# Optimization experiments

Measured on AMD Instinct MI355X. Metric: run time of the kernel, lower is better.

The kernel has to match this reference:

```python
import jax, jax.numpy as jnp
import numpy as np

B, S, IK, IV = 16, 2048, 3, 1
D = IK + IV          # input_size = 4
H = 256              # hidden_size
F = 512              # dim_feedforward
L = 2                # num_layers
EPS = 1e-5


def setup_inputs() -> dict:
    key = jax.random.key(0)
    ks = jax.random.split(key, 16)
    n = jax.random.normal
    inp = {
        'KEY': n(ks[0], (B, S, IK), jnp.float32),
        'VALUE': n(ks[1], (B, S, IV), jnp.float32),
        # per-layer kernel-attention projections (stacked on layer axis)
        'Wq': n(ks[2], (L, D, H), jnp.float32) * 0.1,
        'bq': jnp.zeros((L, H), jnp.float32),
        'Wk': n(ks[3], (L, D, H), jnp.float32) * 0.1,
        'bk': jnp.zeros((L, H), jnp.float32),
        'Wv': n(ks[4], (L, D, H), jnp.float32) * 0.1,
        'bv': jnp.zeros((L, H), jnp.float32),
        'Wo': n(ks[5], (L, H, D), jnp.float32) * 0.1,
        'bo': jnp.zeros((L, D), jnp.float32),
        'bw': jnp.ones((L,), jnp.float32),          # Gaussian kernel bandwidth
        # LayerNorm 1
        'g1': jnp.ones((L, D), jnp.float32),
        'be1': jnp.zeros((L, D), jnp.float32),
        # FFN
        'W1': n(ks[6], (L, D, F), jnp.float32) * 0.1,
        'b1': jnp.zeros((L, F), jnp.float32),
        'W2': n(ks[7], (L, F, D), jnp.float32) * 0.1,
        'b2': jnp.zeros((L, D), jnp.float32),
        # LayerNorm 2
        'g2': jnp.ones((L, D), jnp.float32),
        'be2': jnp.zeros((L, D), jnp.float32),
        # final fc: input_size -> input_v
        'Wfc': n(ks[8], (D, IV), jnp.float32) * 0.1,
        'bfc': jnp.zeros((IV,), jnp.float32),
    }
    return inp


def _layernorm(x, g, b):
    m = x.mean(-1, keepdims=True)
    v = ((x - m) ** 2).mean(-1, keepdims=True)
    return (x - m) * jax.lax.rsqrt(v + EPS) * g + b


def reference(KEY, VALUE, Wq, bq, Wk, bk, Wv, bv, Wo, bo, bw,
              g1, be1, W1, b1, W2, b2, g2, be2, Wfc, bfc):
    # positioning: concat coords and values -> [B, S, D]
    X = jnp.concatenate([KEY, VALUE], axis=-1)
    n_layers = Wq.shape[0]
    for i in range(n_layers):
        # Nadaraya-Watson Gaussian kernel attention (madsnn, type='nwd', kernel='gauss')
        Q = X @ Wq[i] + bq[i]                      # [B,S,H]
        K = X @ Wk[i] + bk[i]                      # [B,S,H]
        V = X @ Wv[i] + bv[i]                      # [B,S,H]
        # pairwise squared distances ||q-k||^2, [B,S,S]
        d2 = ((Q * Q).sum(-1)[:, :, None]
              + (K * K).sum(-1)[:, None, :]
              - 2.0 * jnp.einsum('bqh,bkh->bqk', Q, K))
        attn = jax.nn.softmax(-0.5 * d2 * (bw[i] ** 2), axis=-1)
        attn_out = jnp.einsum('bqk,bkh->bqh', attn, V) @ Wo[i] + bo[i]  # [B,S,D]
        # residual + LayerNorm + FFN + residual + LayerNorm (dropout = identity in eval)
        res = _layernorm(X + attn_out, g1[i], be1[i])
        ff = jax.nn.relu(res @ W1[i] + b1[i]) @ W2[i] + b2[i]
        X = _layernorm(res + ff, g2[i], be2[i])
    return X @ Wfc + bfc                            # [B,S,IV]
```

## Files before the change

kernel.cpp:

```cpp
#include <hip/hip_runtime.h>

#define BB 16
#define SS 2048
#define NTOK (BB*SS)
#define FF 512
#define EPSF 1e-5f

#if __has_builtin(__builtin_amdgcn_exp2f)
#define EXP2F(x) __builtin_amdgcn_exp2f(x)
#else
#define EXP2F(x) exp2f(x)
#endif


__device__ __forceinline__ float wred64(float v) {
#pragma unroll
  for (int m = 32; m > 0; m >>= 1) v += __shfl_xor(v, m, 64);
  return v;
}


__global__ __launch_bounds__(64) void prep_kernel(
    const float* __restrict__ Wq, const float* __restrict__ bq,
    const float* __restrict__ Wk, const float* __restrict__ bk,
    const float* __restrict__ Wv, const float* __restrict__ bv,
    const float* __restrict__ Wo, const float* __restrict__ bw,
    const float* __restrict__ W1, const float* __restrict__ b1,
    const float* __restrict__ W2,
    float* __restrict__ sm, float* __restrict__ w1t)
{
  const int i = blockIdx.x;
  const int lane = threadIdx.x;
  float m4[4][4] = {{0}}, gkk[4][4] = {{0}}, wvo[4][4] = {{0}};
  float akk[4] = {0}, bvo[4] = {0};
  float ck1 = 0.f, ck2 = 0.f;

  for (int h = lane; h < 256; h += 64) {
    float vq[4], vk[4], vv[4], wo4[4];
#pragma unroll
    for (int a = 0; a < 4; ++a) {
      vq[a]  = Wq[(i*4 + a)*256 + h];
      vk[a]  = Wk[(i*4 + a)*256 + h];
      vv[a]  = Wv[(i*4 + a)*256 + h];
      wo4[a] = Wo[(i*256 + h)*4 + a];
    }
    const float bqh = bq[i*256 + h], bkh = bk[i*256 + h], bvh = bv[i*256 + h];
#pragma unroll
    for (int a = 0; a < 4; ++a) {
#pragma unroll
      for (int c = 0; c < 4; ++c) {
        m4[a][c]  = fmaf(vq[a], vk[c], m4[a][c]);
        gkk[a][c] = fmaf(vk[a], vk[c], gkk[a][c]);
        wvo[a][c] = fmaf(vv[a], wo4[c], wvo[a][c]);
      }
      akk[a] = fmaf(vk[a], bqh - bkh, akk[a]);
      bvo[a] = fmaf(bvh, wo4[a], bvo[a]);
    }
    ck1 = fmaf(bqh, bkh, ck1);
    ck2 = fmaf(bkh, bkh, ck2);
  }
#pragma unroll
  for (int a = 0; a < 4; ++a) {
#pragma unroll
    for (int c = 0; c < 4; ++c) {
      m4[a][c]  = wred64(m4[a][c]);
      gkk[a][c] = wred64(gkk[a][c]);
      wvo[a][c] = wred64(wvo[a][c]);
    }
    akk[a] = wred64(akk[a]);
    bvo[a] = wred64(bvo[a]);
  }
  ck1 = wred64(ck1); ck2 = wred64(ck2);

  if (lane == 0) {
    const float bwv = bw[i];
    const float bw2 = bwv * bwv * 1.44269504088896f;
    float* s = sm + i*64;
#pragma unroll
    for (int a = 0; a < 4; ++a) {
#pragma unroll
      for (int c = 0; c < 4; ++c) {
        s[a*4+c]      = bw2 * m4[a][c];
        s[16 + a*4+c] = -0.5f * bw2 * gkk[a][c];
        s[32 + a*4+c] = wvo[a][c];
      }
      s[48+a] = bw2 * akk[a];
      s[52+a] = bvo[a];
    }
    s[56] = bw2 * (ck1 - 0.5f * ck2);
  }
  for (int f = lane; f < FF; f += 64) {
    float* rec = w1t + (i*FF + f)*12;
#pragma unroll
    for (int c = 0; c < 4; ++c) rec[c]   = W1[(i*4 + c)*FF + f];
#pragma unroll
    for (int c = 0; c < 4; ++c) rec[4+c] = W2[(i*FF + f)*4 + c];
    rec[8] = b1[i*FF + f];
    rec[9] = 0.f; rec[10] = 0.f; rec[11] = 0.f;
  }
}

__device__ __forceinline__ void compute_feat(const float x[4], const float* __restrict__ s,
                                             float* __restrict__ featrec)
{
  float P[4], VT[4], tk[4];
#pragma unroll
  for (int a = 0; a < 4; ++a) {
    P[a]  = fmaf(s[a*4+3], x[3], fmaf(s[a*4+2], x[2], fmaf(s[a*4+1], x[1], s[a*4+0]*x[0])));
    tk[a] = fmaf(s[16+a*4+3], x[3], fmaf(s[16+a*4+2], x[2], fmaf(s[16+a*4+1], x[1], s[16+a*4+0]*x[0])));
    VT[a] = s[52+a] + fmaf(s[32+3*4+a], x[3], fmaf(s[32+2*4+a], x[2], fmaf(s[32+1*4+a], x[1], s[32+0*4+a]*x[0])));
  }
  float R = s[56];
#pragma unroll
  for (int a = 0; a < 4; ++a) R = fmaf(tk[a] + s[48+a], x[a], R);
  float4* fp = (float4*)featrec;
  fp[0] = make_float4(P[0], P[1], P[2], P[3]);
  fp[1] = make_float4(VT[0], VT[1], VT[2], VT[3]);
  fp[2] = make_float4(R, 0.f, 0.f, 0.f);
}

__global__ __launch_bounds__(256) void f0_kernel(
    const float* __restrict__ KEY, const float* __restrict__ VALUE,
    const float* __restrict__ sm, float* __restrict__ X0, float* __restrict__ feat)
{
  const int gq = blockIdx.x*256 + threadIdx.x;
  float x[4];
  x[0] = KEY[gq*3 + 0];
  x[1] = KEY[gq*3 + 1];
  x[2] = KEY[gq*3 + 2];
  x[3] = VALUE[gq];
  *(float4*)(X0 + (size_t)gq*4) = make_float4(x[0], x[1], x[2], x[3]);
  float fr[12];
  compute_feat(x, sm, fr);
  float4* fp = (float4*)(feat + (size_t)gq*12);
  fp[0] = ((float4*)fr)[0]; fp[1] = ((float4*)fr)[1]; fp[2] = ((float4*)fr)[2];
}

__global__ __launch_bounds__(256) void attn_kernel(
    const float* __restrict__ feat, const float* __restrict__ X,
    float* __restrict__ part)
{
  __shared__ float smem[512*21];
  const int bid = blockIdx.x;
  const int b = bid >> 5;
  const int r = bid & 31;
  const int qg = r >> 3, kb = r & 7;
  const int qbase = (b << 11) + (qg << 9);
  const int kbase = (b << 11) + (kb << 8);
  const int tid = threadIdx.x;
  const int lane = tid & 63, wave = tid >> 6;

  {
    const float4* src = (const float4*)(feat + (size_t)kbase*12);
    float4* dst = (float4*)smem;
    dst[tid] = src[tid];
    dst[tid + 256] = src[tid + 256];
    dst[tid + 512] = src[tid + 512];
  }

  float xq[8][4], acc[8][5];
#pragma unroll
  for (int j = 0; j < 8; ++j) {
    const float4 xv = *(const float4*)(X + (size_t)(qbase + j*64 + lane)*4);
    xq[j][0] = xv.x; xq[j][1] = xv.y; xq[j][2] = xv.z; xq[j][3] = xv.w;
#pragma unroll
    for (int c = 0; c < 5; ++c) acc[j][c] = 0.f;
  }
  __syncthreads();

  const float* kf = smem + wave*64*12;
#pragma unroll 2
  for (int k = 0; k < 64; ++k) {
    const float* kp = kf + k*12;
    const float4 P  = *(const float4*)kp;
    const float4 VT = *(const float4*)(kp + 4);
    const float R = kp[8];
#pragma unroll
    for (int j = 0; j < 8; ++j) {
      float l = fmaf(xq[j][3], P.w, fmaf(xq[j][2], P.z,
                fmaf(xq[j][1], P.y, fmaf(xq[j][0], P.x, R))));
      const float e = EXP2F(l);
      acc[j][0] = fmaf(e, VT.x, acc[j][0]);
      acc[j][1] = fmaf(e, VT.y, acc[j][1]);
      acc[j][2] = fmaf(e, VT.z, acc[j][2]);
      acc[j][3] = fmaf(e, VT.w, acc[j][3]);
      acc[j][4] += e;
    }
  }
  __syncthreads();
#pragma unroll
  for (int j = 0; j < 8; ++j) {
    float* rr = smem + (j*64 + lane)*21 + wave*5;
    rr[0] = acc[j][0]; rr[1] = acc[j][1]; rr[2] = acc[j][2];
    rr[3] = acc[j][3]; rr[4] = acc[j][4];
  }
  __syncthreads();
  float* pb = part + (size_t)kb * NTOK * 8;
#pragma unroll
  for (int t = 0; t < 2; ++t) {
    const int q = t*256 + tid;
    const float* rr = smem + q*21;
    float s0 = 0.f, s1 = 0.f, s2 = 0.f, s3 = 0.f, s4 = 0.f;
#pragma unroll
    for (int w = 0; w < 4; ++w) {
      s0 += rr[w*5+0]; s1 += rr[w*5+1]; s2 += rr[w*5+2];
      s3 += rr[w*5+3]; s4 += rr[w*5+4];
    }
    float* pp = pb + (size_t)(qbase + q)*8;
    *(float4*)pp = make_float4(s0, s1, s2, s3);
    pp[4] = s4;
  }
}

__device__ __forceinline__ void ln4(const float t[4], const float* __restrict__ g,
                                    const float* __restrict__ b, float r[4])
{
  const float m = 0.25f*(t[0]+t[1]+t[2]+t[3]);
  const float d0 = t[0]-m, d1 = t[1]-m, d2 = t[2]-m, d3 = t[3]-m;
  const float v = 0.25f*(d0*d0 + d1*d1 + d2*d2 + d3*d3);
  const float sc = rsqrtf(v + EPSF);
  r[0] = fmaf(d0*sc, g[0], b[0]);
  r[1] = fmaf(d1*sc, g[1], b[1]);
  r[2] = fmaf(d2*sc, g[2], b[2]);
  r[3] = fmaf(d3*sc, g[3], b[3]);
}

__global__ __launch_bounds__(512) void combine_kernel(
    const float* __restrict__ part, const float* __restrict__ Xin,
    const float* __restrict__ w1t,
    const float* __restrict__ bo, const float* __restrict__ g1, const float* __restrict__ be1,
    const float* __restrict__ b2v, const float* __restrict__ g2, const float* __restrict__ be2,
    const float* __restrict__ smn,
    float* __restrict__ Xout, float* __restrict__ feat,
    const float* __restrict__ Wfc, const float* __restrict__ bfc,
    float* __restrict__ outp, int last)
{
  const int tok = threadIdx.x & 63, fc = threadIdx.x >> 6;
  const int gq = blockIdx.x*64 + tok;
  __shared__ float redp[8][64][5];
  __shared__ float ress[64][4];
  __shared__ float redf[8][64][4];

  {
    const float* pp = part + ((size_t)fc*NTOK + gq)*8;
    const float4 v = *(const float4*)pp;
    redp[fc][tok][0] = v.x; redp[fc][tok][1] = v.y;
    redp[fc][tok][2] = v.z; redp[fc][tok][3] = v.w;
    redp[fc][tok][4] = pp[4];
  }
  __syncthreads();

  if (fc == 0) {
    float acc[5] = {0,0,0,0,0};
#pragma unroll
    for (int k = 0; k < 8; ++k)
#pragma unroll
      for (int c = 0; c < 5; ++c) acc[c] += redp[k][tok][c];
    const float inv = 1.0f / acc[4];
    const float4 xv = *(const float4*)(Xin + (size_t)gq*4);
    float t[4];
    t[0] = xv.x + fmaf(acc[0], inv, bo[0]);
    t[1] = xv.y + fmaf(acc[1], inv, bo[1]);
    t[2] = xv.z + fmaf(acc[2], inv, bo[2]);
    t[3] = xv.w + fmaf(acc[3], inv, bo[3]);
    float r[4];
    ln4(t, g1, be1, r);
    ress[tok][0] = r[0]; ress[tok][1] = r[1]; ress[tok][2] = r[2]; ress[tok][3] = r[3];
  }
  __syncthreads();

  const float r0 = ress[tok][0], r1 = ress[tok][1], r2 = ress[tok][2], r3 = ress[tok][3];
  float fa[4] = {0,0,0,0};
  const float* wt = w1t + (size_t)fc*64*12;
#pragma unroll 4
  for (int f = 0; f < 64; ++f) {
    const float* rec = wt + f*12;
    const float4 w1r = *(const float4*)rec;
    const float4 w2r = *(const float4*)(rec + 4);
    const float b1f = rec[8];
    float h = fmaf(r3, w1r.w, fmaf(r2, w1r.z, fmaf(r1, w1r.y, fmaf(r0, w1r.x, b1f))));
    h = fmaxf(h, 0.f);
    fa[0] = fmaf(h, w2r.x, fa[0]);
    fa[1] = fmaf(h, w2r.y, fa[1]);
    fa[2] = fmaf(h, w2r.z, fa[2]);
    fa[3] = fmaf(h, w2r.w, fa[3]);
  }
  redf[fc][tok][0] = fa[0]; redf[fc][tok][1] = fa[1];
  redf[fc][tok][2] = fa[2]; redf[fc][tok][3] = fa[3];
  __syncthreads();

  if (fc == 0) {
    float t2[4];
#pragma unroll
    for (int c = 0; c < 4; ++c) {
      float s = b2v[c];
#pragma unroll
      for (int k = 0; k < 8; ++k) s += redf[k][tok][c];
      t2[c] = ress[tok][c] + s;
    }
    float y[4];
    ln4(t2, g2, be2, y);
    if (last) {
      outp[gq] = fmaf(y[3], Wfc[3], fmaf(y[2], Wfc[2], fmaf(y[1], Wfc[1], fmaf(y[0], Wfc[0], bfc[0]))));
    } else {
      *(float4*)(Xout + (size_t)gq*4) = make_float4(y[0], y[1], y[2], y[3]);
      float fr[12];
      compute_feat(y, smn, fr);
      float4* fp = (float4*)(feat + (size_t)gq*12);
      fp[0] = ((float4*)fr)[0]; fp[1] = ((float4*)fr)[1]; fp[2] = ((float4*)fr)[2];
    }
  }
}

extern "C" void kernel_launch(void* const* d_in, const int* in_sizes, int n_in,
                              void* d_out, int out_size, void* d_ws, size_t ws_size,
                              hipStream_t stream)
{
  const float* KEY   = (const float*)d_in[0];
  const float* VALUE = (const float*)d_in[1];
  const float* Wq  = (const float*)d_in[2];
  const float* bq  = (const float*)d_in[3];
  const float* Wk  = (const float*)d_in[4];
  const float* bk  = (const float*)d_in[5];
  const float* Wv  = (const float*)d_in[6];
  const float* bv  = (const float*)d_in[7];
  const float* Wo  = (const float*)d_in[8];
  const float* bo  = (const float*)d_in[9];
  const float* bw  = (const float*)d_in[10];
  const float* g1  = (const float*)d_in[11];
  const float* be1 = (const float*)d_in[12];
  const float* W1  = (const float*)d_in[13];
  const float* b1  = (const float*)d_in[14];
  const float* W2  = (const float*)d_in[15];
  const float* b2  = (const float*)d_in[16];
  const float* g2  = (const float*)d_in[17];
  const float* be2 = (const float*)d_in[18];
  const float* Wfc = (const float*)d_in[19];
  const float* bfc = (const float*)d_in[20];
  float* out = (float*)d_out;

  float* w    = (float*)d_ws;
  float* sm   = w;
  float* w1t  = w + 128;
  float* feat = w + 12416;
  float* X0   = w + 405632;
  float* X1   = w + 536704;
  float* part = w + 667776;

  prep_kernel<<<2, 64, 0, stream>>>(Wq, bq, Wk, bk, Wv, bv, Wo, bw, W1, b1, W2, sm, w1t);
  f0_kernel<<<128, 256, 0, stream>>>(KEY, VALUE, sm, X0, feat);

  attn_kernel<<<512, 256, 0, stream>>>(feat, X0, part);
  combine_kernel<<<512, 512, 0, stream>>>(part, X0, w1t,
      bo, g1, be1, b2, g2, be2,
      sm + 64, X1, feat, Wfc, bfc, out, 0);

  attn_kernel<<<512, 256, 0, stream>>>(feat, X1, part);
  combine_kernel<<<512, 512, 0, stream>>>(part, X1, w1t + FF*12,
      bo + 4, g1 + 4, be1 + 4, b2 + 4, g2 + 4, be2 + 4,
      sm, X0, feat, Wfc, bfc, out, 1);
}
```

Before: 191.8 us.

## Compute key features on the fly in attention kernel, merge f0 into prep

Drops the precomputed per-token feature buffer. Each attention block now recomputes its 256 key features from X into shared memory, and the combine kernel no longer writes features. The f0 kernel is folded into prep_kernel, which also packs KEY/VALUE into X0, removing one launch. This trades a small amount of redundant per-block compute for less global memory traffic and one fewer kernel launch.

```diff
diff --git a/kernel.cpp b/kernel.cpp
--- a/kernel.cpp
+++ b/kernel.cpp
@@ -20,16 +20,25 @@
 }
 
 
-__global__ __launch_bounds__(64) void prep_kernel(
+__global__ __launch_bounds__(256) void prep_kernel(
+    const float* __restrict__ KEY, const float* __restrict__ VALUE,
     const float* __restrict__ Wq, const float* __restrict__ bq,
     const float* __restrict__ Wk, const float* __restrict__ bk,
     const float* __restrict__ Wv, const float* __restrict__ bv,
     const float* __restrict__ Wo, const float* __restrict__ bw,
     const float* __restrict__ W1, const float* __restrict__ b1,
     const float* __restrict__ W2,
-    float* __restrict__ sm, float* __restrict__ w1t)
-{
-  const int i = blockIdx.x;
+    float* __restrict__ sm, float* __restrict__ w1t, float* __restrict__ X0)
+{
+  const int bid = blockIdx.x;
+  if (bid < 128) {
+    const int gq = bid*256 + threadIdx.x;
+    *(float4*)(X0 + (size_t)gq*4) =
+        make_float4(KEY[gq*3 + 0], KEY[gq*3 + 1], KEY[gq*3 + 2], VALUE[gq]);
+    return;
+  }
+  const int i = bid - 128;
+  if (threadIdx.x >= 64) return;
   const int lane = threadIdx.x;
   float m4[4][4] = {{0}}, gkk[4][4] = {{0}}, wvo[4][4] = {{0}};
   float akk[4] = {0}, bvo[4] = {0};
@@ -119,25 +128,8 @@
   fp[2] = make_float4(R, 0.f, 0.f, 0.f);
 }
 
-__global__ __launch_bounds__(256) void f0_kernel(
-    const float* __restrict__ KEY, const float* __restrict__ VALUE,
-    const float* __restrict__ sm, float* __restrict__ X0, float* __restrict__ feat)
-{
-  const int gq = blockIdx.x*256 + threadIdx.x;
-  float x[4];
-  x[0] = KEY[gq*3 + 0];
-  x[1] = KEY[gq*3 + 1];
-  x[2] = KEY[gq*3 + 2];
-  x[3] = VALUE[gq];
-  *(float4*)(X0 + (size_t)gq*4) = make_float4(x[0], x[1], x[2], x[3]);
-  float fr[12];
-  compute_feat(x, sm, fr);
-  float4* fp = (float4*)(feat + (size_t)gq*12);
-  fp[0] = ((float4*)fr)[0]; fp[1] = ((float4*)fr)[1]; fp[2] = ((float4*)fr)[2];
-}
-
 __global__ __launch_bounds__(256) void attn_kernel(
-    const float* __restrict__ feat, const float* __restrict__ X,
+    const float* __restrict__ X, const float* __restrict__ sm,
     float* __restrict__ part)
 {
   __shared__ float smem[512*21];
@@ -151,11 +143,14 @@
   const int lane = tid & 63, wave = tid >> 6;
 
   {
-    const float4* src = (const float4*)(feat + (size_t)kbase*12);
-    float4* dst = (float4*)smem;
-    dst[tid] = src[tid];
-    dst[tid + 256] = src[tid + 256];
-    dst[tid + 512] = src[tid + 512];
+    const float4 xk = *(const float4*)(X + (size_t)(kbase + tid)*4);
+    float xr[4] = {xk.x, xk.y, xk.z, xk.w};
+    float fr[12];
+    compute_feat(xr, sm, fr);
+    float* dst = smem + tid*12;
+    ((float4*)dst)[0] = ((float4*)fr)[0];
+    ((float4*)dst)[1] = ((float4*)fr)[1];
+    dst[8] = fr[8];
   }
 
   float xq[8][4], acc[8][5];
@@ -230,8 +225,7 @@
     const float* __restrict__ w1t,
     const float* __restrict__ bo, const float* __restrict__ g1, const float* __restrict__ be1,
     const float* __restrict__ b2v, const float* __restrict__ g2, const float* __restrict__ be2,
-    const float* __restrict__ smn,
-    float* __restrict__ Xout, float* __restrict__ feat,
+    float* __restrict__ Xout,
     const float* __restrict__ Wfc, const float* __restrict__ bfc,
     float* __restrict__ outp, int last)
 {
@@ -304,10 +298,6 @@
       outp[gq] = fmaf(y[3], Wfc[3], fmaf(y[2], Wfc[2], fmaf(y[1], Wfc[1], fmaf(y[0], Wfc[0], bfc[0]))));
     } else {
       *(float4*)(Xout + (size_t)gq*4) = make_float4(y[0], y[1], y[2], y[3]);
-      float fr[12];
-      compute_feat(y, smn, fr);
-      float4* fp = (float4*)(feat + (size_t)gq*12);
-      fp[0] = ((float4*)fr)[0]; fp[1] = ((float4*)fr)[1]; fp[2] = ((float4*)fr)[2];
     }
   }
 }
@@ -342,21 +332,20 @@
   float* w    = (float*)d_ws;
   float* sm   = w;
   float* w1t  = w + 128;
-  float* feat = w + 12416;
-  float* X0   = w + 405632;
-  float* X1   = w + 536704;
-  float* part = w + 667776;
-
-  prep_kernel<<<2, 64, 0, stream>>>(Wq, bq, Wk, bk, Wv, bv, Wo, bw, W1, b1, W2, sm, w1t);
-  f0_kernel<<<128, 256, 0, stream>>>(KEY, VALUE, sm, X0, feat);
-
-  attn_kernel<<<512, 256, 0, stream>>>(feat, X0, part);
+  float* X0   = w + 12416;
+  float* X1   = w + 143488;
+  float* part = w + 274560;
+
+  prep_kernel<<<130, 256, 0, stream>>>(KEY, VALUE, Wq, bq, Wk, bk, Wv, bv, Wo, bw,
+                                       W1, b1, W2, sm, w1t, X0);
+
+  attn_kernel<<<512, 256, 0, stream>>>(X0, sm, part);
   combine_kernel<<<512, 512, 0, stream>>>(part, X0, w1t,
       bo, g1, be1, b2, g2, be2,
-      sm + 64, X1, feat, Wfc, bfc, out, 0);
-
-  attn_kernel<<<512, 256, 0, stream>>>(feat, X1, part);
+      X1, Wfc, bfc, out, 0);
+
+  attn_kernel<<<512, 256, 0, stream>>>(X1, sm + 64, part);
   combine_kernel<<<512, 512, 0, stream>>>(part, X1, w1t + FF*12,
       bo + 4, g1 + 4, be1 + 4, b2 + 4, g2 + 4, be2 + 4,
-      sm, X0, feat, Wfc, bfc, out, 1);
-}
+      X0, Wfc, bfc, out, 1);
+}
```

New measurement: 186.8 us. -2.6%, faster.
